# Kernel optimization log

Hardware: AMD Instinct MI355X
Metric: run time of the kernel (lower is better)

The kernel has to match this reference:

```python
import jax, jax.numpy as jnp
import numpy as np

N, E, NB = 50000, 100000, 6          # nodes, directed messages, max neighbors
NF, BF, H, DEPTH = 98, 6, 256, 6     # node feat, bond feat, hidden, depth
EF = NF + BF                          # edge_fdim: hmess = [fnode[src], bond_feats]


def setup_inputs() -> dict:
    key = jax.random.key(0)
    ks = jax.random.split(key, 12)
    s = lambda fan: np.float32(1.0 / np.sqrt(fan))
    return {
        "fnode": jax.random.normal(ks[0], (N, NF), jnp.float32),
        "fmess_idx": jax.random.randint(ks[1], (E, 2), 0, N),
        "fmess_feat": jax.random.normal(ks[2], (E, BF), jnp.float32),
        "agraph": jax.random.randint(ks[3], (N, NB), 0, E),
        "bgraph": jax.random.randint(ks[4], (E, NB), 0, E),
        "Wz": jax.random.normal(ks[5], (3, EF + H, H), jnp.float32) * s(EF + H),
        "bz": jnp.zeros((3, H), jnp.float32),
        "Wr": jax.random.normal(ks[6], (3, EF, H), jnp.float32) * s(EF),
        "Ur": jax.random.normal(ks[7], (3, H, H), jnp.float32) * s(H),
        "bur": jnp.zeros((3, H), jnp.float32),
        "Wh": jax.random.normal(ks[8], (3, EF + H, H), jnp.float32) * s(EF + H),
        "bh": jnp.zeros((3, H), jnp.float32),
        "Wo": jax.random.normal(ks[9], (3, NF + H, H), jnp.float32) * s(NF + H),
        "bo": jnp.zeros((3, H), jnp.float32),
    }


def _mpn(hnode, hmess, agraph, bgraph, Wz, bz, Wr, Ur, bur, Wh, bh, Wo, bo):
    # One MPNLayer: depth-unrolled message GRU over bgraph, then node readout via agraph.
    e_mask = jnp.ones((hmess.shape[0], 1), hmess.dtype).at[0, 0].set(0.0)  # msg 0 = padding
    r1 = hmess @ Wr  # W_r(fmess), loop-invariant  [E,H]

    def step(h, _):
        h_nei = h[bgraph]                                    # [E,NB,H] gather inbound msgs
        sum_h = h_nei.sum(axis=1)
        z = jax.nn.sigmoid(jnp.concatenate([hmess, sum_h], axis=1) @ Wz + bz)
        r = jax.nn.sigmoid(r1[:, None, :] + h_nei @ Ur + bur)  # [E,NB,H]
        sum_gh = (r * h_nei).sum(axis=1)
        pre_h = jnp.tanh(jnp.concatenate([hmess, sum_gh], axis=1) @ Wh + bh)
        return ((1.0 - z) * sum_h + z * pre_h) * e_mask, None

    h0 = jnp.zeros((hmess.shape[0], bz.shape[0]), hmess.dtype)
    h, _ = jax.lax.scan(step, h0, None, length=DEPTH)
    nei = h[agraph].sum(axis=1)                              # [N,H]
    node_h = jax.nn.relu(jnp.concatenate([hnode, nei], axis=1) @ Wo + bo)
    n_mask = jnp.ones((hnode.shape[0], 1), hnode.dtype).at[0, 0].set(0.0)  # node 0 = padding
    return node_h * n_mask


def reference(fnode, fmess_idx, fmess_feat, agraph, bgraph,
              Wz, bz, Wr, Ur, bur, Wh, bh, Wo, bo):
    # embed_graph: gather source-node features, concat with bond features
    hmess = jnp.concatenate([fnode[fmess_idx[:, 0]], fmess_feat], axis=1)  # [E,EF]
    run = jax.vmap(lambda a, b, c, d, e, f, g, hh, i: _mpn(
        fnode, hmess, agraph, bgraph, a, b, c, d, e, f, g, hh, i))
    qkv = run(Wz, bz, Wr, Ur, bur, Wh, bh, Wo, bo)           # [3,N,H]: Q/K/V encoders batched
    return (qkv[0], qkv[1], qkv[2])
```

## Files before the change

kernel.cpp:

```cpp
#include <hip/hip_runtime.h>


#define NE 100000
#define NEP 100032
#define NN 50000

typedef unsigned short u16;
typedef short short8 __attribute__((ext_vector_type(8)));
typedef float f32x4 __attribute__((ext_vector_type(4)));
typedef unsigned short u16x4 __attribute__((ext_vector_type(4)));

__device__ __forceinline__ float b2f(u16 u) {
  union { unsigned int i; float f; } v; v.i = ((unsigned int)u) << 16; return v.f;
}
__device__ __forceinline__ u16 f2b(float f) {
  union { float f; unsigned int i; } v; v.f = f;
  unsigned int b = v.i;
  b += 0x7FFFu + ((b >> 16) & 1u);
  return (u16)(b >> 16);
}
__device__ __forceinline__ float sigm(float x) { return 1.0f / (1.0f + __expf(-x)); }
__device__ __forceinline__ float tanh_f(float x) { return 2.0f / (1.0f + __expf(-2.0f * x)) - 1.0f; }
__device__ __forceinline__ f32x4 mfma16(short8 a, short8 b, f32x4 c) {
  return __builtin_amdgcn_mfma_f32_16x16x32_bf16(a, b, c, 0, 0, 0);
}

__global__ void pack_wpre(const float* __restrict__ Wr, const float* __restrict__ Wz,
                          const float* __restrict__ Wh, u16* __restrict__ dst) {
  const int g = blockIdx.y;
  const int p = blockIdx.x * 256 + threadIdx.x;
  const int j = p & 7, l = (p >> 3) & 63, q = p >> 9;
  const int nb = q % 48, s = q / 48;
  const int k = 32 * s + 8 * (l >> 4) + j;
  const int n = 16 * nb + (l & 15);
  float v = 0.f;
  if (k < 104) {
    if (n < 256)      v = Wr[((size_t)g * 104 + k) * 256 + n];
    else if (n < 512) v = Wz[((size_t)g * 360 + k) * 256 + (n - 256)];
    else              v = Wh[((size_t)g * 360 + k) * 256 + (n - 512)];
  }
  dst[(size_t)g * 98304 + p] = f2b(v);
}

__global__ void pack_wgate(const float* __restrict__ Wz, const float* __restrict__ Wh,
                           u16* __restrict__ dst) {
  const int g = blockIdx.y;
  const int p = blockIdx.x * 256 + threadIdx.x;
  const int j = p & 7, l = (p >> 3) & 63, q = p >> 9;
  const int nb = q % 32, s = q / 32;
  const int k = 32 * s + 8 * (l >> 4) + j;
  const int n = 16 * nb + (l & 15);
  float v = (n < 256) ? Wz[((size_t)g * 360 + 104 + k) * 256 + n]
                      : Wh[((size_t)g * 360 + 104 + k) * 256 + (n - 256)];
  dst[(size_t)g * 131072 + p] = f2b(v);
}

__global__ void pack_ur(const float* __restrict__ Ur, u16* __restrict__ dst) {
  const int g = blockIdx.y;
  const int p = blockIdx.x * 256 + threadIdx.x;
  const int j = p & 7, l = (p >> 3) & 63, q = p >> 9;
  const int nb = q % 16, s = q / 16;
  const int k = 32 * s + 8 * (l >> 4) + j;
  const int n = 16 * nb + (l & 15);
  dst[(size_t)g * 65536 + p] = f2b(Ur[((size_t)g * 256 + k) * 256 + n]);
}

__global__ void pack_wo(const float* __restrict__ Wo, u16* __restrict__ dst) {
  const int g = blockIdx.y;
  const int p = blockIdx.x * 256 + threadIdx.x;
  const int j = p & 7, l = (p >> 3) & 63, q = p >> 9;
  const int nb = q % 16, s = q / 16;
  const int k = 32 * s + 8 * (l >> 4) + j;
  const int n = 16 * nb + (l & 15);
  float v = 0.f;
  if (k < 98)        v = Wo[((size_t)g * 354 + k) * 256 + n];
  else if (k >= 128) v = Wo[((size_t)g * 354 + (k - 30)) * 256 + n];
  dst[(size_t)g * 98304 + p] = f2b(v);
}

__global__ void embed_hmess_f(const float* __restrict__ fnode, const int* __restrict__ fmess_idx,
                              const float* __restrict__ fmess_feat, u16* __restrict__ hmF) {
  const int e = blockIdx.x * 2 + (threadIdx.x >> 7);
  const int c = threadIdx.x & 127;
  const int src = fmess_idx[e * 2];
  float v = 0.f;
  if (c < 98)       v = fnode[(size_t)src * 98 + c];
  else if (c < 104) v = fmess_feat[(size_t)e * 6 + (c - 98)];
  hmF[(size_t)(e >> 4) * 2048 + ((c >> 5) * 64 + (e & 15) + 16 * ((c >> 3) & 3)) * 8 + (c & 7)] = f2b(v);
}

__global__ void embed_fnode(const float* __restrict__ fnode, u16* __restrict__ fnp) {
  const int n = blockIdx.x * 2 + (threadIdx.x >> 7);
  const int c = threadIdx.x & 127;
  float v = (c < 98) ? fnode[(size_t)n * 98 + c] : 0.f;
  fnp[(size_t)n * 128 + c] = f2b(v);
}

__global__ __launch_bounds__(256)
void pre_gemm_t(const u16* __restrict__ hmF, const u16* __restrict__ Wpre,
                const float* __restrict__ bur, const float* __restrict__ bz,
                const float* __restrict__ bh, u16* __restrict__ r1b,
                u16* __restrict__ zpF, u16* __restrict__ hpF) {
  const int tid = threadIdx.x, wave = tid >> 6, lane = tid & 63;
  const int row0 = lane & 15, kq = lane >> 4;
  const int e0 = blockIdx.x * 32;
  const int cchunk = blockIdx.y;
  f32x4 acc[2][4];
#pragma unroll
  for (int i = 0; i < 2; ++i)
#pragma unroll
    for (int n = 0; n < 4; ++n) { acc[i][n][0]=0.f; acc[i][n][1]=0.f; acc[i][n][2]=0.f; acc[i][n][3]=0.f; }
#pragma unroll
  for (int kc = 0; kc < 4; ++kc) {
    short8 bf[2];
#pragma unroll
    for (int ef = 0; ef < 2; ++ef)
      bf[ef] = *(const short8*)(hmF + (size_t)((e0 >> 4) + ef) * 2048 + (size_t)(kc * 64 + lane) * 8);
#pragma unroll
    for (int nf = 0; nf < 4; ++nf) {
      const int nb = cchunk * 16 + wave * 4 + nf;
      short8 wf = *(const short8*)(Wpre + ((size_t)(kc * 48 + nb) * 64 + lane) * 8);
      acc[0][nf] = mfma16(wf, bf[0], acc[0][nf]);
      acc[1][nf] = mfma16(wf, bf[1], acc[1][nf]);
    }
  }
  const float* bias = (cchunk == 0) ? bur : (cchunk == 1 ? bz : bh);
  u16* dstF = (cchunk == 1) ? zpF : hpF;
#pragma unroll
  for (int ef = 0; ef < 2; ++ef)
#pragma unroll
    for (int nf = 0; nf < 4; ++nf) {
      const int n256 = wave * 64 + nf * 16 + kq * 4;
      const int e = e0 + ef * 16 + row0;
      u16x4 o;
#pragma unroll
      for (int v = 0; v < 4; ++v) o[v] = f2b(acc[ef][nf][v] + bias[n256 + v]);
      if (cchunk == 0) {
        *(u16x4*)(r1b + (size_t)e * 256 + n256) = o;
      } else {
        *(u16x4*)(dstF + ((size_t)((e0 >> 4) + ef) * 16 + (wave * 4 + nf)) * 256 + lane * 4) = o;
      }
    }
}

__global__ __launch_bounds__(512, 4)
void mpn_fused(const u16* __restrict__ HBin, u16* __restrict__ HBout,
               const u16* __restrict__ r1b, const int* __restrict__ bgraph,
               const u16* __restrict__ zpF, const u16* __restrict__ hpF,
               const u16* __restrict__ Wgate, const u16* __restrict__ Urp) {
  __shared__ __align__(16) u16 sF[32768];
  const int tid = threadIdx.x;
  const int wn = tid >> 6, lane = tid & 63;
  const int row0 = lane & 15, kq = lane >> 4;
  const int e0 = blockIdx.x * 64;

  const int c0 = 4 * lane;
  const int offc = ((c0 >> 5) * 64 + 16 * ((c0 >> 3) & 3)) * 8 + (c0 & 7);
#pragma unroll 2
  for (int rr = 0; rr < 8; ++rr) {
    const int r = wn * 8 + rr;
    const int e = e0 + r;
    float sh[4] = {0.f, 0.f, 0.f, 0.f}, sg[4] = {0.f, 0.f, 0.f, 0.f};
    if (e < NE) {
      const u16x4 r1v = *(const u16x4*)(r1b + (size_t)e * 256 + c0);
      int idx[6];
#pragma unroll
      for (int k = 0; k < 6; ++k) idx[k] = bgraph[e * 6 + k];
      u16x4 hv[6], huv[6];
#pragma unroll
      for (int k = 0; k < 6; ++k) {
        const u16* rowp = HBin + (size_t)idx[k] * 512;
        hv[k]  = *(const u16x4*)(rowp + c0);
        huv[k] = *(const u16x4*)(rowp + 256 + c0);
      }
#pragma unroll
      for (int k = 0; k < 6; ++k)
#pragma unroll
        for (int j = 0; j < 4; ++j) {
          const float h  = b2f(hv[k][j]);
          const float rg = sigm(b2f(r1v[j]) + b2f(huv[k][j]));
          sh[j] += h;
          sg[j] += rg * h;
        }
    }
    u16x4 o0, o1;
#pragma unroll
    for (int j = 0; j < 4; ++j) { o0[j] = f2b(sh[j]); o1[j] = f2b(sg[j]); }
    const int off = (r >> 4) * 4096 + offc + (r & 15) * 8;
    *(u16x4*)(sF + off) = o0;
    *(u16x4*)(sF + 16384 + off) = o1;
  }
  __syncthreads();

  f32x4 aZ[2][4], aH[2][4];
#pragma unroll
  for (int nf = 0; nf < 2; ++nf)
#pragma unroll
    for (int ef = 0; ef < 4; ++ef) {
      aZ[nf][ef][0]=0.f; aZ[nf][ef][1]=0.f; aZ[nf][ef][2]=0.f; aZ[nf][ef][3]=0.f;
      aH[nf][ef][0]=0.f; aH[nf][ef][1]=0.f; aH[nf][ef][2]=0.f; aH[nf][ef][3]=0.f;
    }
#pragma unroll
  for (int kc = 0; kc < 8; ++kc) {
    short8 wz0 = *(const short8*)(Wgate + ((size_t)(kc * 32 + wn * 2 + 0) * 64 + lane) * 8);
    short8 wz1 = *(const short8*)(Wgate + ((size_t)(kc * 32 + wn * 2 + 1) * 64 + lane) * 8);
    short8 wh0 = *(const short8*)(Wgate + ((size_t)(kc * 32 + 16 + wn * 2 + 0) * 64 + lane) * 8);
    short8 wh1 = *(const short8*)(Wgate + ((size_t)(kc * 32 + 16 + wn * 2 + 1) * 64 + lane) * 8);
#pragma unroll
    for (int ef = 0; ef < 4; ++ef) {
      short8 bsh = *(const short8*)(sF + ef * 4096 + (kc * 64 + lane) * 8);
      short8 bsg = *(const short8*)(sF + 16384 + ef * 4096 + (kc * 64 + lane) * 8);
      aZ[0][ef] = mfma16(wz0, bsh, aZ[0][ef]);
      aZ[1][ef] = mfma16(wz1, bsh, aZ[1][ef]);
      aH[0][ef] = mfma16(wh0, bsg, aH[0][ef]);
      aH[1][ef] = mfma16(wh1, bsg, aH[1][ef]);
    }
  }

  u16x4 hq[2][4];
#pragma unroll
  for (int nf = 0; nf < 2; ++nf) {
    const int lp = row0 + 16 * (nf * 2 + (kq >> 1));
    const int jo = 4 * (kq & 1);
    const int nc = wn * 2 + nf;
#pragma unroll
    for (int ef = 0; ef < 4; ++ef) {
      const int ev = (e0 + ef * 16) < NE;
      const int e  = e0 + ef * 16 + row0;
      const u16x4 shv = *(const u16x4*)(sF + ef * 4096 + (wn * 64 + lp) * 8 + jo);
      const size_t tb = ((size_t)((e0 >> 4) + ef) * 16 + nc) * 256 + lane * 4;
      const u16x4 zp4 = *(const u16x4*)(zpF + tb);
      const u16x4 hp4 = *(const u16x4*)(hpF + tb);
#pragma unroll
      for (int v = 0; v < 4; ++v) {
        const float z  = sigm(b2f(zp4[v]) + aZ[nf][ef][v]);
        const float ph = tanh_f(b2f(hp4[v]) + aH[nf][ef][v]);
        float hf = (1.0f - z) * b2f(shv[v]) + z * ph;
        if (e == 0 || !ev) hf = 0.f;
        hq[nf][ef][v] = f2b(hf);
      }
    }
  }
  __syncthreads();

#pragma unroll
  for (int nf = 0; nf < 2; ++nf) {
    const int lp = row0 + 16 * (nf * 2 + (kq >> 1));
    const int jo = 4 * (kq & 1);
#pragma unroll
    for (int ef = 0; ef < 4; ++ef)
      *(u16x4*)(sF + 16384 + ef * 4096 + (wn * 64 + lp) * 8 + jo) = hq[nf][ef];
  }
  __syncthreads();

  f32x4 aU[2][4];
#pragma unroll
  for (int nf = 0; nf < 2; ++nf)
#pragma unroll
    for (int ef = 0; ef < 4; ++ef) { aU[nf][ef][0]=0.f; aU[nf][ef][1]=0.f; aU[nf][ef][2]=0.f; aU[nf][ef][3]=0.f; }
#pragma unroll
  for (int kc = 0; kc < 8; ++kc) {
    short8 u0 = *(const short8*)(Urp + ((size_t)(kc * 16 + wn * 2 + 0) * 64 + lane) * 8);
    short8 u1 = *(const short8*)(Urp + ((size_t)(kc * 16 + wn * 2 + 1) * 64 + lane) * 8);
#pragma unroll
    for (int ef = 0; ef < 4; ++ef) {
      short8 hb = *(const short8*)(sF + 16384 + ef * 4096 + (kc * 64 + lane) * 8);
      aU[0][ef] = mfma16(u0, hb, aU[0][ef]);
      aU[1][ef] = mfma16(u1, hb, aU[1][ef]);
    }
  }

  {
    const int r = tid >> 3;
    const int e = e0 + r;
    if (e < NE) {
#pragma unroll
      for (int it = 0; it < 4; ++it) {
        const int c = (tid & 7) * 8 + it * 64;
        const short8 val = *(const short8*)(sF + 16384 + (r >> 4) * 4096 +
                           (((c >> 5) * 64 + (r & 15) + 16 * ((c >> 3) & 3)) * 8));
        *(short8*)(HBout + (size_t)e * 512 + c) = val;
      }
    }
  }
#pragma unroll
  for (int nf = 0; nf < 2; ++nf) {
    const int lp = row0 + 16 * (nf * 2 + (kq >> 1));
    const int jo = 4 * (kq & 1);
#pragma unroll
    for (int ef = 0; ef < 4; ++ef) {
      u16x4 uq;
#pragma unroll
      for (int v = 0; v < 4; ++v) uq[v] = f2b(aU[nf][ef][v]);
      *(u16x4*)(sF + ef * 4096 + (wn * 64 + lp) * 8 + jo) = uq;
    }
  }
  __syncthreads();

  {
    const int r = tid >> 3;
    const int e = e0 + r;
    if (e < NE) {
#pragma unroll
      for (int it = 0; it < 4; ++it) {
        const int c = (tid & 7) * 8 + it * 64;
        const short8 val = *(const short8*)(sF + (r >> 4) * 4096 +
                           (((c >> 5) * 64 + (r & 15) + 16 * ((c >> 3) & 3)) * 8));
        *(short8*)(HBout + (size_t)e * 512 + 256 + c) = val;
      }
    }
  }
}

__global__ __launch_bounds__(512, 4)
void step0(u16* __restrict__ HB, const u16* __restrict__ zpF, const u16* __restrict__ hpF,
           const u16* __restrict__ Urp) {
  __shared__ __align__(16) u16 sHn[16384];
  const int tid = threadIdx.x;
  const int wn = tid >> 6, lane = tid & 63;
  const int row0 = lane & 15, kq = lane >> 4;
  const int e0 = blockIdx.x * 64;

#pragma unroll
  for (int nf = 0; nf < 2; ++nf) {
    const int lp = row0 + 16 * (nf * 2 + (kq >> 1));
    const int jo = 4 * (kq & 1);
    const int nc = wn * 2 + nf;
#pragma unroll
    for (int ef = 0; ef < 4; ++ef) {
      const int ev = (e0 + ef * 16) < NE;
      const int e  = e0 + ef * 16 + row0;
      const size_t tb = ((size_t)((e0 >> 4) + ef) * 16 + nc) * 256 + lane * 4;
      const u16x4 zp4 = *(const u16x4*)(zpF + tb);
      const u16x4 hp4 = *(const u16x4*)(hpF + tb);
      u16x4 hq;
#pragma unroll
      for (int v = 0; v < 4; ++v) {
        float hf = sigm(b2f(zp4[v])) * tanh_f(b2f(hp4[v]));
        if (e == 0 || !ev) hf = 0.f;
        hq[v] = f2b(hf);
      }
      *(u16x4*)(sHn + (size_t)ef * 4096 + (size_t)(wn * 64 + lp) * 8 + jo) = hq;
    }
  }
  __syncthreads();

  f32x4 aU[2][4];
#pragma unroll
  for (int nf = 0; nf < 2; ++nf)
#pragma unroll
    for (int ef = 0; ef < 4; ++ef) { aU[nf][ef][0]=0.f; aU[nf][ef][1]=0.f; aU[nf][ef][2]=0.f; aU[nf][ef][3]=0.f; }
#pragma unroll
  for (int kc = 0; kc < 8; ++kc) {
    short8 u0 = *(const short8*)(Urp + ((size_t)(kc * 16 + wn * 2 + 0) * 64 + lane) * 8);
    short8 u1 = *(const short8*)(Urp + ((size_t)(kc * 16 + wn * 2 + 1) * 64 + lane) * 8);
#pragma unroll
    for (int ef = 0; ef < 4; ++ef) {
      short8 hb = *(const short8*)(sHn + (size_t)ef * 4096 + (size_t)(kc * 64 + lane) * 8);
      aU[0][ef] = mfma16(u0, hb, aU[0][ef]);
      aU[1][ef] = mfma16(u1, hb, aU[1][ef]);
    }
  }
  {
    const int r = tid >> 3;
    const int e = e0 + r;
    if (e < NE) {
#pragma unroll
      for (int it = 0; it < 4; ++it) {
        const int c = (tid & 7) * 8 + it * 64;
        const short8 val = *(const short8*)(sHn + (size_t)(r >> 4) * 4096 +
                           (size_t)(((c >> 5) * 64 + (r & 15) + 16 * ((c >> 3) & 3)) * 8));
        *(short8*)(HB + (size_t)e * 512 + c) = val;
      }
    }
  }
  __syncthreads();
#pragma unroll
  for (int nf = 0; nf < 2; ++nf) {
    const int lp = row0 + 16 * (nf * 2 + (kq >> 1));
    const int jo = 4 * (kq & 1);
#pragma unroll
    for (int ef = 0; ef < 4; ++ef) {
      u16x4 uq;
#pragma unroll
      for (int v = 0; v < 4; ++v) uq[v] = f2b(aU[nf][ef][v]);
      *(u16x4*)(sHn + (size_t)ef * 4096 + (size_t)(wn * 64 + lp) * 8 + jo) = uq;
    }
  }
  __syncthreads();
  {
    const int r = tid >> 3;
    const int e = e0 + r;
    if (e < NE) {
#pragma unroll
      for (int it = 0; it < 4; ++it) {
        const int c = (tid & 7) * 8 + it * 64;
        const short8 val = *(const short8*)(sHn + (size_t)(r >> 4) * 4096 +
                           (size_t)(((c >> 5) * 64 + (r & 15) + 16 * ((c >> 3) & 3)) * 8));
        *(short8*)(HB + (size_t)e * 512 + 256 + c) = val;
      }
    }
  }
}

__global__ __launch_bounds__(256)
void readout(const u16* __restrict__ HB, const u16* __restrict__ fnp,
             const int* __restrict__ agraph, const u16* __restrict__ Wop,
             const float* __restrict__ bo, float* __restrict__ out) {
  __shared__ __align__(16) u16 sN[32][264];
  const int tid = threadIdx.x, wave = tid >> 6, lane = tid & 63;
  const int n0 = blockIdx.x * 32;
  const int row0 = lane & 15, kq = lane >> 4;

#pragma unroll 2
  for (int rr = 0; rr < 8; ++rr) {
    const int r = wave * 8 + rr;
    const int n = n0 + r;
    float s4[4] = {0.f, 0.f, 0.f, 0.f};
    if (n < NN) {
#pragma unroll
      for (int k = 0; k < 6; ++k) {
        const int idx = agraph[n * 6 + k];
        const u16x4 hv = *(const u16x4*)(HB + (size_t)idx * 512 + 4 * lane);
#pragma unroll
        for (int j = 0; j < 4; ++j) s4[j] += b2f(hv[j]);
      }
    }
#pragma unroll
    for (int j = 0; j < 4; ++j) sN[r][4 * lane + j] = f2b(s4[j]);
  }
  __syncthreads();

  f32x4 acc[2][4];
#pragma unroll
  for (int i = 0; i < 2; ++i)
#pragma unroll
    for (int n = 0; n < 4; ++n) { acc[i][n][0]=0.f; acc[i][n][1]=0.f; acc[i][n][2]=0.f; acc[i][n][3]=0.f; }
  const int ra = min(n0 + row0, NN - 1);
  const int rb = min(n0 + 16 + row0, NN - 1);
#pragma unroll
  for (int s = 0; s < 12; ++s) {
    short8 a0, a1;
    if (s < 4) {
      a0 = *(const short8*)(fnp + (size_t)ra * 128 + s * 32 + kq * 8);
      a1 = *(const short8*)(fnp + (size_t)rb * 128 + s * 32 + kq * 8);
    } else {
      a0 = *(const short8*)&sN[row0][(s - 4) * 32 + kq * 8];
      a1 = *(const short8*)&sN[row0 + 16][(s - 4) * 32 + kq * 8];
    }
#pragma unroll
    for (int ni = 0; ni < 4; ++ni) {
      short8 b = *(const short8*)(Wop + ((size_t)(s * 16 + wave * 4 + ni) * 64 + lane) * 8);
      acc[0][ni] = mfma16(a0, b, acc[0][ni]);
      acc[1][ni] = mfma16(a1, b, acc[1][ni]);
    }
  }
#pragma unroll
  for (int mi = 0; mi < 2; ++mi)
#pragma unroll
    for (int ni = 0; ni < 4; ++ni)
#pragma unroll
      for (int v = 0; v < 4; ++v) {
        const int m = mi * 16 + kq * 4 + v;
        const int col = wave * 64 + ni * 16 + row0;
        const int n = n0 + m;
        if (n < NN) {
          float val = fmaxf(acc[mi][ni][v] + bo[col], 0.f);
          if (n == 0) val = 0.f;
          out[(size_t)n * 256 + col] = val;
        }
      }
}

extern "C" void kernel_launch(void* const* d_in, const int* in_sizes, int n_in,
                              void* d_out, int out_size, void* d_ws, size_t ws_size,
                              hipStream_t stream) {
  const float* fnode      = (const float*)d_in[0];
  const int*   fmess_idx  = (const int*)d_in[1];
  const float* fmess_feat = (const float*)d_in[2];
  const int*   agraph     = (const int*)d_in[3];
  const int*   bgraph     = (const int*)d_in[4];
  const float* Wz         = (const float*)d_in[5];
  const float* bz         = (const float*)d_in[6];
  const float* Wr         = (const float*)d_in[7];
  const float* Ur         = (const float*)d_in[8];
  const float* bur        = (const float*)d_in[9];
  const float* Wh         = (const float*)d_in[10];
  const float* bh         = (const float*)d_in[11];
  const float* Wo         = (const float*)d_in[12];
  const float* bo         = (const float*)d_in[13];
  float* out = (float*)d_out;

  char* ws = (char*)d_ws;
  size_t off = 0;
  auto carve = [&](size_t bytes) -> char* {
    char* p = ws + off;
    off += (bytes + 511) & ~(size_t)511;
    return p;
  };
  u16* HB0  = (u16*)carve((size_t)NEP * 512 * 2);
  u16* HB1  = (u16*)carve((size_t)NEP * 512 * 2);
  u16* r1b  = (u16*)carve((size_t)NEP * 256 * 2);
  u16* zpF  = (u16*)carve((size_t)NEP * 256 * 2);
  u16* hpF  = (u16*)carve((size_t)NEP * 256 * 2);
  u16* hmF  = (u16*)carve((size_t)NEP * 128 * 2);
  u16* fnp  = (u16*)carve((size_t)NN * 128 * 2);
  u16* wpre = (u16*)carve((size_t)3 * 98304 * 2);
  u16* wgate= (u16*)carve((size_t)3 * 131072 * 2);
  u16* urp  = (u16*)carve((size_t)3 * 65536 * 2);
  u16* wop  = (u16*)carve((size_t)3 * 98304 * 2);
  if (off > ws_size) return;

  pack_wpre <<<dim3(384, 3), 256, 0, stream>>>(Wr, Wz, Wh, wpre);
  pack_wgate<<<dim3(512, 3), 256, 0, stream>>>(Wz, Wh, wgate);
  pack_ur   <<<dim3(256, 3), 256, 0, stream>>>(Ur, urp);
  pack_wo   <<<dim3(384, 3), 256, 0, stream>>>(Wo, wop);
  embed_hmess_f<<<NE / 2, 256, 0, stream>>>(fnode, fmess_idx, fmess_feat, hmF);
  embed_fnode<<<NN / 2, 256, 0, stream>>>(fnode, fnp);

  for (int g = 0; g < 3; ++g) {
    pre_gemm_t<<<dim3(NEP / 32, 3), 256, 0, stream>>>(
        hmF, wpre + (size_t)g * 98304, bur + g * 256, bz + g * 256, bh + g * 256,
        r1b, zpF, hpF);
    const u16* wgate_g = wgate + (size_t)g * 131072;
    const u16* urp_g   = urp + (size_t)g * 65536;
    step0<<<NEP / 64, 512, 0, stream>>>(HB0, zpF, hpF, urp_g);
    u16* bufs[2] = {HB0, HB1};
    int cur = 0;
    for (int d = 1; d < 6; ++d) {
      mpn_fused<<<NEP / 64, 512, 0, stream>>>(bufs[cur], bufs[1 - cur], r1b, bgraph,
                                              zpF, hpF, wgate_g, urp_g);
      cur ^= 1;
    }
    readout<<<(NN + 31) / 32, 256, 0, stream>>>(
        bufs[cur], fnp, agraph, wop + (size_t)g * 98304, bo + g * 256, out + (size_t)g * NN * 256);
  }
}
```

Before: 3.306 ms.

## Restructure gather phase to 16-byte fragment-layout loads with nontemporal streams

```diff
diff --git a/kernel.cpp b/kernel.cpp
--- a/kernel.cpp
+++ b/kernel.cpp
@@ -9,6 +9,8 @@
 typedef short short8 __attribute__((ext_vector_type(8)));
 typedef float f32x4 __attribute__((ext_vector_type(4)));
 typedef unsigned short u16x4 __attribute__((ext_vector_type(4)));
+typedef unsigned int u32x4 __attribute__((ext_vector_type(4)));
+typedef unsigned int u32x2 __attribute__((ext_vector_type(2)));
 
 __device__ __forceinline__ float b2f(u16 u) {
   union { unsigned int i; float f; } v; v.i = ((unsigned int)u) << 16; return v.f;
@@ -19,10 +21,23 @@
   b += 0x7FFFu + ((b >> 16) & 1u);
   return (u16)(b >> 16);
 }
+__device__ __forceinline__ unsigned cvtpk(float lo, float hi) {
+  unsigned r;
+  asm("v_cvt_pk_bf16_f32 %0, %1, %2" : "=v"(r) : "v"(lo), "v"(hi));
+  return r;
+}
 __device__ __forceinline__ float sigm(float x) { return 1.0f / (1.0f + __expf(-x)); }
 __device__ __forceinline__ float tanh_f(float x) { return 2.0f / (1.0f + __expf(-2.0f * x)) - 1.0f; }
 __device__ __forceinline__ f32x4 mfma16(short8 a, short8 b, f32x4 c) {
   return __builtin_amdgcn_mfma_f32_16x16x32_bf16(a, b, c, 0, 0, 0);
+}
+__device__ __forceinline__ short8 ldnt16(const u16* p) {
+  u32x4 t = __builtin_nontemporal_load((const u32x4*)p);
+  union { u32x4 u; short8 s; } v; v.u = t; return v.s;
+}
+__device__ __forceinline__ u16x4 ldnt8(const u16* p) {
+  u32x2 t = __builtin_nontemporal_load((const u32x2*)p);
+  union { u32x2 u; u16x4 s; } v; v.u = t; return v.s;
 }
 
 __global__ void pack_wpre(const float* __restrict__ Wr, const float* __restrict__ Wz,
@@ -99,7 +114,7 @@
 __global__ __launch_bounds__(256)
 void pre_gemm_t(const u16* __restrict__ hmF, const u16* __restrict__ Wpre,
                 const float* __restrict__ bur, const float* __restrict__ bz,
-                const float* __restrict__ bh, u16* __restrict__ r1b,
+                const float* __restrict__ bh, u16* __restrict__ r1F,
                 u16* __restrict__ zpF, u16* __restrict__ hpF) {
   const int tid = threadIdx.x, wave = tid >> 6, lane = tid & 63;
   const int row0 = lane & 15, kq = lane >> 4;
@@ -131,12 +146,12 @@
 #pragma unroll
     for (int nf = 0; nf < 4; ++nf) {
       const int n256 = wave * 64 + nf * 16 + kq * 4;
-      const int e = e0 + ef * 16 + row0;
       u16x4 o;
 #pragma unroll
       for (int v = 0; v < 4; ++v) o[v] = f2b(acc[ef][nf][v] + bias[n256 + v]);
       if (cchunk == 0) {
-        *(u16x4*)(r1b + (size_t)e * 256 + n256) = o;
+        *(u16x4*)(r1F + (size_t)((e0 >> 4) + ef) * 4096 +
+                  (((n256 >> 5) * 64 + row0 + 16 * ((n256 >> 3) & 3)) * 8 + (n256 & 7))) = o;
       } else {
         *(u16x4*)(dstF + ((size_t)((e0 >> 4) + ef) * 16 + (wave * 4 + nf)) * 256 + lane * 4) = o;
       }
@@ -145,7 +160,7 @@
 
 __global__ __launch_bounds__(512, 4)
 void mpn_fused(const u16* __restrict__ HBin, u16* __restrict__ HBout,
-               const u16* __restrict__ r1b, const int* __restrict__ bgraph,
+               const u16* __restrict__ r1F, const int* __restrict__ bgraph,
                const u16* __restrict__ zpF, const u16* __restrict__ hpF,
                const u16* __restrict__ Wgate, const u16* __restrict__ Urp) {
   __shared__ __align__(16) u16 sF[32768];
@@ -154,41 +169,50 @@
   const int row0 = lane & 15, kq = lane >> 4;
   const int e0 = blockIdx.x * 64;
 
-  const int c0 = 4 * lane;
-  const int offc = ((c0 >> 5) * 64 + 16 * ((c0 >> 3) & 3)) * 8 + (c0 & 7);
-#pragma unroll 2
-  for (int rr = 0; rr < 8; ++rr) {
-    const int r = wn * 8 + rr;
-    const int e = e0 + r;
-    float sh[4] = {0.f, 0.f, 0.f, 0.f}, sg[4] = {0.f, 0.f, 0.f, 0.f};
-    if (e < NE) {
-      const u16x4 r1v = *(const u16x4*)(r1b + (size_t)e * 256 + c0);
-      int idx[6];
+  {
+    const int chunk = wn >> 1;
+    const int kh = (wn & 1) * 4;
+    const int e = e0 + chunk * 16 + (lane & 15);
+    const int oct = lane >> 4;
+    const bool ev = (e < NE);
+    int idx[6];
+    if (ev) {
 #pragma unroll
       for (int k = 0; k < 6; ++k) idx[k] = bgraph[e * 6 + k];
-      u16x4 hv[6], huv[6];
-#pragma unroll
-      for (int k = 0; k < 6; ++k) {
-        const u16* rowp = HBin + (size_t)idx[k] * 512;
-        hv[k]  = *(const u16x4*)(rowp + c0);
-        huv[k] = *(const u16x4*)(rowp + 256 + c0);
-      }
-#pragma unroll
-      for (int k = 0; k < 6; ++k)
-#pragma unroll
-        for (int j = 0; j < 4; ++j) {
-          const float h  = b2f(hv[k][j]);
-          const float rg = sigm(b2f(r1v[j]) + b2f(huv[k][j]));
-          sh[j] += h;
-          sg[j] += rg * h;
+    }
+#pragma unroll
+    for (int ki = 0; ki < 4; ++ki) {
+      const int kc = kh + ki;
+      float sh8[8] = {0.f,0.f,0.f,0.f,0.f,0.f,0.f,0.f};
+      float sg8[8] = {0.f,0.f,0.f,0.f,0.f,0.f,0.f,0.f};
+      if (ev) {
+        const short8 r1v = ldnt16(r1F + ((size_t)(e0 >> 4) + chunk) * 4096 + (size_t)(kc * 64 + lane) * 8);
+        float r1c[8];
+#pragma unroll
+        for (int j = 0; j < 8; ++j) r1c[j] = b2f((u16)r1v[j]);
+#pragma unroll
+        for (int k = 0; k < 6; ++k) {
+          const u16* rowp = HBin + (size_t)idx[k] * 512 + kc * 32 + oct * 8;
+          const short8 hv = *(const short8*)rowp;
+          const short8 uv = *(const short8*)(rowp + 256);
+#pragma unroll
+          for (int j = 0; j < 8; ++j) {
+            const float h  = b2f((u16)hv[j]);
+            const float rg = sigm(r1c[j] + b2f((u16)uv[j]));
+            sh8[j] += h;
+            sg8[j] += rg * h;
+          }
         }
-    }
-    u16x4 o0, o1;
-#pragma unroll
-    for (int j = 0; j < 4; ++j) { o0[j] = f2b(sh[j]); o1[j] = f2b(sg[j]); }
-    const int off = (r >> 4) * 4096 + offc + (r & 15) * 8;
-    *(u16x4*)(sF + off) = o0;
-    *(u16x4*)(sF + 16384 + off) = o1;
+      }
+      u32x4 o0, o1;
+#pragma unroll
+      for (int q = 0; q < 4; ++q) {
+        o0[q] = cvtpk(sh8[2 * q], sh8[2 * q + 1]);
+        o1[q] = cvtpk(sg8[2 * q], sg8[2 * q + 1]);
+      }
+      *(u32x4*)(sF + chunk * 4096 + (kc * 64 + lane) * 8) = o0;
+      *(u32x4*)(sF + 16384 + chunk * 4096 + (kc * 64 + lane) * 8) = o1;
+    }
   }
   __syncthreads();
 
@@ -229,16 +253,21 @@
       const int e  = e0 + ef * 16 + row0;
       const u16x4 shv = *(const u16x4*)(sF + ef * 4096 + (wn * 64 + lp) * 8 + jo);
       const size_t tb = ((size_t)((e0 >> 4) + ef) * 16 + nc) * 256 + lane * 4;
-      const u16x4 zp4 = *(const u16x4*)(zpF + tb);
-      const u16x4 hp4 = *(const u16x4*)(hpF + tb);
+      const u16x4 zp4 = ldnt8(zpF + tb);
+      const u16x4 hp4 = ldnt8(hpF + tb);
+      float hf[4];
 #pragma unroll
       for (int v = 0; v < 4; ++v) {
         const float z  = sigm(b2f(zp4[v]) + aZ[nf][ef][v]);
         const float ph = tanh_f(b2f(hp4[v]) + aH[nf][ef][v]);
-        float hf = (1.0f - z) * b2f(shv[v]) + z * ph;
-        if (e == 0 || !ev) hf = 0.f;
-        hq[nf][ef][v] = f2b(hf);
-      }
+        float h = (1.0f - z) * b2f(shv[v]) + z * ph;
+        if (e == 0 || !ev) h = 0.f;
+        hf[v] = h;
+      }
+      union { unsigned w[2]; u16x4 q; } pk;
+      pk.w[0] = cvtpk(hf[0], hf[1]);
+      pk.w[1] = cvtpk(hf[2], hf[3]);
+      hq[nf][ef] = pk.q;
     }
   }
   __syncthreads();
@@ -289,10 +318,10 @@
     const int jo = 4 * (kq & 1);
 #pragma unroll
     for (int ef = 0; ef < 4; ++ef) {
-      u16x4 uq;
-#pragma unroll
-      for (int v = 0; v < 4; ++v) uq[v] = f2b(aU[nf][ef][v]);
-      *(u16x4*)(sF + ef * 4096 + (wn * 64 + lp) * 8 + jo) = uq;
+      union { unsigned w[2]; u16x4 q; } pk;
+      pk.w[0] = cvtpk(aU[nf][ef][0], aU[nf][ef][1]);
+      pk.w[1] = cvtpk(aU[nf][ef][2], aU[nf][ef][3]);
+      *(u16x4*)(sF + ef * 4096 + (wn * 64 + lp) * 8 + jo) = pk.q;
     }
   }
   __syncthreads();
@@ -331,8 +360,8 @@
       const int ev = (e0 + ef * 16) < NE;
       const int e  = e0 + ef * 16 + row0;
       const size_t tb = ((size_t)((e0 >> 4) + ef) * 16 + nc) * 256 + lane * 4;
-      const u16x4 zp4 = *(const u16x4*)(zpF + tb);
-      const u16x4 hp4 = *(const u16x4*)(hpF + tb);
+      const u16x4 zp4 = ldnt8(zpF + tb);
+      const u16x4 hp4 = ldnt8(hpF + tb);
       u16x4 hq;
 #pragma unroll
       for (int v = 0; v < 4; ++v) {
@@ -500,7 +529,7 @@
   };
   u16* HB0  = (u16*)carve((size_t)NEP * 512 * 2);
   u16* HB1  = (u16*)carve((size_t)NEP * 512 * 2);
-  u16* r1b  = (u16*)carve((size_t)NEP * 256 * 2);
+  u16* r1F  = (u16*)carve((size_t)NEP * 256 * 2);
   u16* zpF  = (u16*)carve((size_t)NEP * 256 * 2);
   u16* hpF  = (u16*)carve((size_t)NEP * 256 * 2);
   u16* hmF  = (u16*)carve((size_t)NEP * 128 * 2);
@@ -521,14 +550,14 @@
   for (int g = 0; g < 3; ++g) {
     pre_gemm_t<<<dim3(NEP / 32, 3), 256, 0, stream>>>(
         hmF, wpre + (size_t)g * 98304, bur + g * 256, bz + g * 256, bh + g * 256,
-        r1b, zpF, hpF);
+        r1F, zpF, hpF);
     const u16* wgate_g = wgate + (size_t)g * 131072;
     const u16* urp_g   = urp + (size_t)g * 65536;
     step0<<<NEP / 64, 512, 0, stream>>>(HB0, zpF, hpF, urp_g);
     u16* bufs[2] = {HB0, HB1};
     int cur = 0;
     for (int d = 1; d < 6; ++d) {
-      mpn_fused<<<NEP / 64, 512, 0, stream>>>(bufs[cur], bufs[1 - cur], r1b, bgraph,
+      mpn_fused<<<NEP / 64, 512, 0, stream>>>(bufs[cur], bufs[1 - cur], r1F, bgraph,
                                               zpF, hpF, wgate_g, urp_g);
       cur ^= 1;
     }
```

Result: slower. 3.918 ms (+18.5%).
